# Performance work log

Hardware: AMD Instinct MI355X
Metric: run time of the kernel (lower is better)

## Reference

```python
import jax, jax.numpy as jnp
import numpy as np

B, T, DIM, H, BUCKET = 4, 4096, 1024, 16, 64
E = DIM // H          # head dim = 64
U = T // BUCKET       # number of buckets = 64
EPS = 1e-6


def setup_inputs() -> dict:
    key = jax.random.key(0)
    ks = jax.random.split(key, 5)
    scale = 1.0 / np.sqrt(DIM)
    return {
        "x": jax.random.normal(ks[0], (B, T, DIM), dtype=jnp.float32),
        "Wq": jax.random.normal(ks[1], (DIM, DIM), dtype=jnp.float32) * scale,
        "Wk": jax.random.normal(ks[2], (DIM, DIM), dtype=jnp.float32) * scale,
        "Wv": jax.random.normal(ks[3], (DIM, DIM), dtype=jnp.float32) * scale,
        "Wo": jax.random.normal(ks[4], (DIM, DIM), dtype=jnp.float32) * scale,
        "bo": jnp.zeros((DIM,), dtype=jnp.float32),
    }


def _causal_linear_attn(q, k, v):
    # q, k, v: [b, h, t, e]; psi(k) = elu(k) + 1; q softmaxed over feature dim
    q = jax.nn.softmax(q, axis=-1)
    k = jax.nn.elu(k) + 1.0
    bucket = lambda x: x.reshape(*x.shape[:-2], U, BUCKET, E)  # [b,h,u,n,e]
    b_q, b_k, b_v = bucket(q), bucket(k), bucket(v)
    # cumulative key sums per bucket: [b,h,u,d]
    b_k_cumsum = jnp.cumsum(b_k.sum(axis=-2), axis=2)
    # per-bucket context then cumulative over buckets: [b,h,u,d,e]
    context = jnp.einsum("bhund,bhune->bhude", b_k, b_v)
    context = jnp.cumsum(context, axis=2)
    context = context / (b_k_cumsum[..., None] + EPS)
    # shift by one bucket (blindspot): bucket u sees context through bucket u-1
    context = jnp.concatenate(
        [jnp.zeros_like(context[:, :, :1]), context[:, :, :-1]], axis=2
    )
    attn = jnp.einsum("bhund,bhude->bhune", b_q, context)
    return attn.reshape(q.shape)  # [b,h,t,e]


def reference(x, Wq, Wk, Wv, Wo, bo):
    b, t, _ = x.shape
    q = x @ Wq
    k = x @ Wk
    v = x @ Wv
    merge = lambda z: z.reshape(b, t, H, E).transpose(0, 2, 1, 3)  # [b,h,t,e]
    attn = _causal_linear_attn(merge(q), merge(k), merge(v))
    out = attn.transpose(0, 2, 1, 3).reshape(b, t, DIM)
    return out @ Wo + bo
```

## Files before the change

### kernel.cpp

```cpp
#include <hip/hip_runtime.h>


#define T_LEN 4096
#define DIMN  1024
#define NHEAD 16
#define NB    4
#define MROWS (NB * T_LEN)

typedef float f32x4 __attribute__((ext_vector_type(4)));
typedef short s16x8 __attribute__((ext_vector_type(8)));
typedef short s16x4 __attribute__((ext_vector_type(4)));
using u16 = unsigned short;

__device__ __forceinline__ u16 f2bf(float f) {
  unsigned int u = __float_as_uint(f);
  u += 0x7fffu + ((u >> 16) & 1u);
  return (u16)(u >> 16);
}
__device__ __forceinline__ float bf2f(u16 h) {
  return __uint_as_float(((unsigned int)h) << 16);
}
__device__ __forceinline__ int swz16k(int off) {
  return off ^ (((off >> 7) & 3) << 4);
}

__global__ __launch_bounds__(256) void cvt_all_kern(const float* __restrict__ x,
                                                    const float* __restrict__ W0,
                                                    const float* __restrict__ W1,
                                                    const float* __restrict__ W2,
                                                    const float* __restrict__ W3,
                                                    u16* __restrict__ WT,
                                                    u16* __restrict__ xb) {
  __shared__ float tile[64][65];
  const int tid = threadIdx.x;
  if (blockIdx.x < 1024) {
    const int blk = blockIdx.x & 255;
    const int sel = blockIdx.x >> 8;
    const float* W = (sel == 0) ? W0 : (sel == 1) ? W1 : (sel == 2) ? W2 : W3;
    u16* dst = WT + (size_t)sel * DIMN * DIMN;
    const int k0 = (blk >> 4) << 6;
    const int n0 = (blk & 15) << 6;
    const int r = tid >> 6;
    const int c = tid & 63;
#pragma unroll
    for (int i = 0; i < 16; ++i) {
      int row = (i << 2) + r;
      tile[row][c] = W[(size_t)(k0 + row) * DIMN + n0 + c];
    }
    __syncthreads();
#pragma unroll
    for (int i = 0; i < 16; ++i) {
      int row = (i << 2) + r;
      dst[(size_t)(n0 + row) * DIMN + k0 + c] = f2bf(tile[c][row]);
    }
  } else {
    size_t i = ((size_t)(blockIdx.x - 1024) * 256 + tid) * 4;
    f32x4 v = *(const f32x4*)(x + i);
    s16x4 o;
    o.x = (short)f2bf(v.x); o.y = (short)f2bf(v.y);
    o.z = (short)f2bf(v.z); o.w = (short)f2bf(v.w);
    *(s16x4*)(xb + i) = o;
  }
}

__global__ __launch_bounds__(512, 4) void gemm_qkv(
    const u16* __restrict__ A, const u16* __restrict__ Bt,
    u16* __restrict__ dq, u16* __restrict__ dk, u16* __restrict__ dv) {
  constexpr int K = 1024;
  constexpr int BNT = 12;
  constexpr int NT = K / 32;
  __shared__ char lds[73728];

  const int tid = threadIdx.x;
  const int l = tid & 63;
  const int w = tid >> 6;
  const int wm = w >> 2;
  const int wn = w & 3;

  const int xcd = (int)blockIdx.x & 7;
  const int idx = (int)blockIdx.x >> 3;
  const int g = idx / (4 * BNT);
  const int r2 = idx % (4 * BNT);
  const int bn = r2 >> 2;
  const int bm = xcd * 16 + g * 4 + (r2 & 3);
  const size_t arow0 = (size_t)bm * 128;
  const size_t brow0 = (size_t)bn * 256;

  int lrow[2], lcol[2];
#pragma unroll
  for (int i = 0; i < 2; ++i) {
    int lg2 = swz16k((i * 512 + tid) * 16);
    lrow[i] = lg2 >> 6;
    lcol[i] = (lg2 & 63) >> 1;
  }

  const int fr = l & 15;
  const int kswz = (((l >> 4) << 4)) ^ ((((fr >> 1) & 3)) << 4);

  auto STAGE = [&](int buf, int matsel, int tt) {
    const int kbase = (tt & (NT - 1)) * 32;
#pragma unroll
    for (int i = 0; i < 2; ++i) {
      if (matsel == 0 && i == 1) break;
      const u16* src = (matsel == 0)
          ? A  + (arow0 + (size_t)lrow[i]) * K + kbase + lcol[i]
          : Bt + (brow0 + (size_t)lrow[i]) * K + kbase + lcol[i];
      char* dst = lds + (buf * 24576 + matsel * 8192 + (i * 512 + tid) * 16);
      __builtin_amdgcn_global_load_lds(
          (__attribute__((address_space(1))) const void*)src,
          (__attribute__((address_space(3))) void*)dst, 16, 0, 0);
    }
  };
  auto LDA = [&](int buf, int rowb) -> s16x8 {
    return *(const s16x8*)(lds + buf * 24576 + rowb * 64 + kswz);
  };
  auto LDB = [&](int buf, int rowb) -> s16x8 {
    return *(const s16x8*)(lds + buf * 24576 + 8192 + rowb * 64 + kswz);
  };

  f32x4 acc[4][4];
#pragma unroll
  for (int i = 0; i < 4; ++i)
#pragma unroll
    for (int j = 0; j < 4; ++j) acc[i][j] = {0.f, 0.f, 0.f, 0.f};

  STAGE(0, 0, 0); STAGE(0, 1, 0);
  STAGE(1, 0, 1); STAGE(1, 1, 1);
  asm volatile("s_waitcnt vmcnt(3)" ::: "memory");
  __builtin_amdgcn_sched_barrier(0);
  __builtin_amdgcn_s_barrier();

  const int amb = wm * 64;
  const int bnb = wn * 64;
  s16x8 af[4], bf[4];

  int bufR = 0, bufW = 2;
#pragma unroll 1
  for (int t = 0; t < NT; ++t) {
    STAGE(bufW, 0, t + 2);
    STAGE(bufW, 1, t + 2);
#pragma unroll
    for (int i = 0; i < 4; ++i) af[i] = LDA(bufR, amb + i * 16 + fr);
#pragma unroll
    for (int i = 0; i < 4; ++i) bf[i] = LDB(bufR, bnb + i * 16 + fr);
    __builtin_amdgcn_s_setprio(1);
#pragma unroll
    for (int mi = 0; mi < 4; ++mi)
#pragma unroll
      for (int ni = 0; ni < 4; ++ni)
        acc[mi][ni] = __builtin_amdgcn_mfma_f32_16x16x32_bf16(
            af[mi], bf[ni], acc[mi][ni], 0, 0, 0);
    __builtin_amdgcn_s_setprio(0);
    asm volatile("s_waitcnt vmcnt(3)" ::: "memory");
    __builtin_amdgcn_sched_barrier(0);
    __builtin_amdgcn_s_barrier();
    bufR = (bufR == 2) ? 0 : bufR + 1;
    bufW = (bufW == 2) ? 0 : bufW + 1;
  }

  asm volatile("s_waitcnt vmcnt(0) lgkmcnt(0)" ::: "memory");
  __builtin_amdgcn_sched_barrier(0);
  __builtin_amdgcn_s_barrier();

  const int r0 = (l >> 4) << 2;
  const int c0 = l & 15;
  const int mat = bn >> 2;
  if (mat == 0) {
    u16* dst = dq;
    const size_t colbase = (size_t)(bn & 3) * 256 + (size_t)wn * 64;
#pragma unroll
    for (int mi = 0; mi < 4; ++mi) {
#pragma unroll
      for (int j = 0; j < 4; ++j) {
        float v0 = acc[mi][0][j], v1 = acc[mi][1][j];
        float v2 = acc[mi][2][j], v3 = acc[mi][3][j];
        float m = fmaxf(fmaxf(v0, v1), fmaxf(v2, v3));
#pragma unroll
        for (int off = 1; off < 16; off <<= 1) m = fmaxf(m, __shfl_xor(m, off));
        float e0 = __expf(v0 - m), e1 = __expf(v1 - m);
        float e2 = __expf(v2 - m), e3 = __expf(v3 - m);
        float s = e0 + e1 + e2 + e3;
#pragma unroll
        for (int off = 1; off < 16; off <<= 1) s += __shfl_xor(s, off);
        float inv = 1.f / s;
        const size_t row = arow0 + wm * 64 + mi * 16 + r0 + j;
        u16* p = dst + row * DIMN + colbase + c0;
        p[0]  = f2bf(e0 * inv); p[16] = f2bf(e1 * inv);
        p[32] = f2bf(e2 * inv); p[48] = f2bf(e3 * inv);
      }
    }
  } else {
    u16* dst = (mat == 1) ? dk : dv;
    u16* lt = (u16*)lds;
#pragma unroll
    for (int mi = 0; mi < 4; ++mi) {
      const int tl = wm * 64 + mi * 16 + r0;
#pragma unroll
      for (int ni = 0; ni < 4; ++ni) {
        const int cl = wn * 64 + ni * 16 + c0;
        s16x4 o;
#pragma unroll
        for (int j = 0; j < 4; ++j) {
          float v = acc[mi][ni][j];
          float r = (mat == 1) ? (v > 0.f ? v + 1.f : __expf(v)) : v;
          o[j] = (short)f2bf(r);
        }
        *(s16x4*)&lt[cl * 132 + tl] = o;
      }
    }
    __builtin_amdgcn_s_barrier();
    const int colb = (bn & 3) * 256;
    const int bb = (int)(arow0 >> 12);
    const int t0 = (int)(arow0 & 4095);
#pragma unroll
    for (int i = 0; i < 8; ++i) {
      const int chunk = i * 512 + tid;
      const int cl = chunk >> 4;
      const int toct = (chunk & 15) * 8;
      s16x8 vv = *(const s16x8*)&lt[cl * 132 + toct];
      const int col = colb + cl;
      const int h = col >> 6, d = col & 63;
      *(s16x8*)&dst[((size_t)((bb * 16 + h) * 64 + d)) * 4096 + t0 + toct] = vv;
    }
  }
}

__global__ __launch_bounds__(512, 2) void gemm_o(
    const u16* __restrict__ A, const u16* __restrict__ Bt,
    float* __restrict__ dO, const float* __restrict__ bias) {
  constexpr int K = 1024;
  constexpr int NT = K / 32;
  extern __shared__ char lds[];

  const int tid = threadIdx.x;
  const int l = tid & 63;
  const int w = tid >> 6;
  const int wm = w >> 2;
  const int wn = w & 3;

  const int xcd = (int)blockIdx.x & 7;
  const int idx = (int)blockIdx.x >> 3;
  const int bm = xcd * 16 + (idx & 15);
  const int bn = idx >> 4;
  const size_t arow0 = (size_t)bm * 128;
  const size_t brow0 = (size_t)bn * 512;

  int lrowA, lcolA, lrowB[4], lcolB[4];
  {
    int lg2 = swz16k(tid * 16);
    lrowA = lg2 >> 6; lcolA = (lg2 & 63) >> 1;
#pragma unroll
    for (int i = 0; i < 4; ++i) {
      int lb = swz16k((i * 512 + tid) * 16);
      lrowB[i] = lb >> 6; lcolB[i] = (lb & 63) >> 1;
    }
  }

  const int fr = l & 15;
  const int kswz = (((l >> 4) << 4)) ^ ((((fr >> 1) & 3)) << 4);

  auto STAGE = [&](int buf, int tt) {
    const int kbase = (tt & (NT - 1)) * 32;
    {
      const u16* src = A + (arow0 + (size_t)lrowA) * K + kbase + lcolA;
      char* dst = lds + (buf * 40960 + tid * 16);
      __builtin_amdgcn_global_load_lds(
          (__attribute__((address_space(1))) const void*)src,
          (__attribute__((address_space(3))) void*)dst, 16, 0, 0);
    }
#pragma unroll
    for (int i = 0; i < 4; ++i) {
      const u16* src = Bt + (brow0 + (size_t)lrowB[i]) * K + kbase + lcolB[i];
      char* dst = lds + (buf * 40960 + 8192 + (i * 512 + tid) * 16);
      __builtin_amdgcn_global_load_lds(
          (__attribute__((address_space(1))) const void*)src,
          (__attribute__((address_space(3))) void*)dst, 16, 0, 0);
    }
  };
  auto LDA = [&](int buf, int rowb) -> s16x8 {
    return *(const s16x8*)(lds + buf * 40960 + rowb * 64 + kswz);
  };
  auto LDB = [&](int buf, int rowb) -> s16x8 {
    return *(const s16x8*)(lds + buf * 40960 + 8192 + rowb * 64 + kswz);
  };

  f32x4 acc[4][8];
#pragma unroll
  for (int i = 0; i < 4; ++i)
#pragma unroll
    for (int j = 0; j < 8; ++j) acc[i][j] = {0.f, 0.f, 0.f, 0.f};

  STAGE(0, 0);
  STAGE(1, 1);
  asm volatile("s_waitcnt vmcnt(5)" ::: "memory");
  __builtin_amdgcn_sched_barrier(0);
  __builtin_amdgcn_s_barrier();

  const int amb = wm * 64;
  const int bnb = wn * 128;
  s16x8 af[4], bf[8];

  int bufR = 0, bufW = 2;
#pragma unroll 1
  for (int t = 0; t < NT; ++t) {
    STAGE(bufW, t + 2);
#pragma unroll
    for (int i = 0; i < 4; ++i) af[i] = LDA(bufR, amb + i * 16 + fr);
#pragma unroll
    for (int i = 0; i < 8; ++i) bf[i] = LDB(bufR, bnb + i * 16 + fr);
    __builtin_amdgcn_s_setprio(1);
#pragma unroll
    for (int mi = 0; mi < 4; ++mi)
#pragma unroll
      for (int ni = 0; ni < 8; ++ni)
        acc[mi][ni] = __builtin_amdgcn_mfma_f32_16x16x32_bf16(
            af[mi], bf[ni], acc[mi][ni], 0, 0, 0);
    __builtin_amdgcn_s_setprio(0);
    asm volatile("s_waitcnt vmcnt(5)" ::: "memory");
    __builtin_amdgcn_sched_barrier(0);
    __builtin_amdgcn_s_barrier();
    bufR = (bufR == 2) ? 0 : bufR + 1;
    bufW = (bufW == 2) ? 0 : bufW + 1;
  }

  const int r0 = (l >> 4) << 2;
  const int c0 = l & 15;
#pragma unroll
  for (int mi = 0; mi < 4; ++mi)
#pragma unroll
    for (int ni = 0; ni < 8; ++ni) {
      const size_t col = brow0 + (size_t)wn * 128 + ni * 16 + c0;
      const float bv = bias[col];
#pragma unroll
      for (int j = 0; j < 4; ++j) {
        const size_t row = arow0 + wm * 64 + mi * 16 + r0 + j;
        dO[row * DIMN + col] = acc[mi][ni][j] + bv;
      }
    }
}

__global__ __launch_bounds__(512) void mid_fused_kern(const u16* __restrict__ kT,
                                                      const u16* __restrict__ vT,
                                                      const u16* __restrict__ qb,
                                                      u16* __restrict__ attn) {
  __shared__ u16 cprev[2][16][72];
  const int tid = threadIdx.x;
  const int l = tid & 63;
  const int w = tid >> 6;
  const int ws = w & 3;
  const bool isCtx = w < 4;
  const int fr = l & 15;
  const int lg = l >> 4;

  const int bid = (int)blockIdx.x;
  const int xcd = bid & 7;
  const int slot = bid >> 3;
  const int bh = xcd * 8 + (slot >> 2);
  const int eg = slot & 3;
  const int b = bh >> 4, h = bh & 15;

  const size_t kvbase = (size_t)bh * 64 * 4096;
  const size_t qrow0 = (size_t)b * T_LEN;

  if (isCtx) {
#pragma unroll
    for (int j = 0; j < 4; ++j) cprev[0][lg * 4 + j][ws * 16 + fr] = 0;
  }
  __syncthreads();

  if (isCtx) {
    auto LV = [&](int u, int kk) -> s16x8 {
      return *(const s16x8*)&vT[kvbase + (size_t)(eg * 16 + fr) * 4096 +
                                u * 64 + kk * 32 + lg * 8];
    };
    auto LK = [&](int u, int kk) -> s16x8 {
      return *(const s16x8*)&kT[kvbase + (size_t)(ws * 16 + fr) * 4096 +
                                u * 64 + kk * 32 + lg * 8];
    };
    f32x4 cacc = {0.f, 0.f, 0.f, 0.f};
    float ksum = 0.f;
    s16x8 vA0 = LV(0, 0), vA1 = LV(0, 1);
    s16x8 kB0 = LK(0, 0), kB1 = LK(0, 1);
#pragma unroll 1
    for (int u = 0; u < 64; ++u) {
      const s16x8 cvA0 = vA0, cvA1 = vA1, ckB0 = kB0, ckB1 = kB1;
      if (u < 63) {
        vA0 = LV(u + 1, 0); vA1 = LV(u + 1, 1);
        kB0 = LK(u + 1, 0); kB1 = LK(u + 1, 1);
      }
      cacc = __builtin_amdgcn_mfma_f32_16x16x32_bf16(cvA0, ckB0, cacc, 0, 0, 0);
      cacc = __builtin_amdgcn_mfma_f32_16x16x32_bf16(cvA1, ckB1, cacc, 0, 0, 0);
      float s = 0.f;
#pragma unroll
      for (int j = 0; j < 8; ++j)
        s += bf2f((u16)ckB0[j]) + bf2f((u16)ckB1[j]);
      s += __shfl_xor(s, 16);
      s += __shfl_xor(s, 32);
      ksum += s;
      const float inv = 1.f / (ksum + 1e-6f);
      u16* pp = &cprev[(u + 1) & 1][lg * 4][ws * 16 + fr];
#pragma unroll
      for (int j = 0; j < 4; ++j) pp[j * 72] = f2bf(cacc[j] * inv);
      __syncthreads();
    }
  } else {
    auto LQ = [&](int u, int kk) -> s16x8 {
      return *(const s16x8*)&qb[(qrow0 + u * 64 + ws * 16 + fr) * DIMN +
                                (size_t)h * 64 + kk * 32 + lg * 8];
    };
    s16x8 qA0 = LQ(0, 0), qA1 = LQ(0, 1);
#pragma unroll 1
    for (int u = 0; u < 64; ++u) {
      const s16x8 cqA0 = qA0, cqA1 = qA1;
      if (u < 63) { qA0 = LQ(u + 1, 0); qA1 = LQ(u + 1, 1); }
      s16x8 cB0 = *(const s16x8*)&cprev[u & 1][fr][lg * 8];
      s16x8 cB1 = *(const s16x8*)&cprev[u & 1][fr][32 + lg * 8];
      f32x4 aacc = {0.f, 0.f, 0.f, 0.f};
      aacc = __builtin_amdgcn_mfma_f32_16x16x32_bf16(cqA0, cB0, aacc, 0, 0, 0);
      aacc = __builtin_amdgcn_mfma_f32_16x16x32_bf16(cqA1, cB1, aacc, 0, 0, 0);
      const size_t arow = qrow0 + (size_t)u * 64 + ws * 16 + lg * 4;
#pragma unroll
      for (int j = 0; j < 4; ++j)
        attn[(arow + j) * DIMN + (size_t)h * 64 + eg * 16 + fr] = f2bf(aacc[j]);
      __syncthreads();
    }
  }
}

extern "C" void kernel_launch(void* const* d_in, const int* in_sizes, int n_in,
                              void* d_out, int out_size, void* d_ws, size_t ws_size,
                              hipStream_t stream) {
  const float* x  = (const float*)d_in[0];
  const float* Wq = (const float*)d_in[1];
  const float* Wk = (const float*)d_in[2];
  const float* Wv = (const float*)d_in[3];
  const float* Wo = (const float*)d_in[4];
  const float* bo = (const float*)d_in[5];
  float* out = (float*)d_out;

  constexpr size_t SZ_XB = (size_t)MROWS * DIMN * 2;
  constexpr size_t SZ_WT = (size_t)DIMN * DIMN * 2;
  char* ws = (char*)d_ws;
  u16*   xb   = (u16*)(ws);
  u16*   wqT  = (u16*)(ws + SZ_XB);
  u16*   woT  = (u16*)(ws + SZ_XB + 3 * SZ_WT);
  u16*   qb   = (u16*)(ws + SZ_XB + 4 * SZ_WT);
  u16*   kT   = (u16*)(ws + 2 * SZ_XB + 4 * SZ_WT);
  u16*   vT   = (u16*)(ws + 3 * SZ_XB + 4 * SZ_WT);
  u16*   attn = xb;

  (void)hipFuncSetAttribute((const void*)gemm_o,
                            hipFuncAttributeMaxDynamicSharedMemorySize, 122880);

  cvt_all_kern<<<1024 + MROWS * DIMN / 1024, 256, 0, stream>>>(x, Wq, Wk, Wv, Wo,
                                                               wqT, xb);

  gemm_qkv<<<1536, 512, 0, stream>>>(xb, wqT, qb, kT, vT);

  mid_fused_kern<<<256, 512, 0, stream>>>(kT, vT, qb, attn);

  gemm_o<<<256, 512, 122880, stream>>>(attn, woT, out, bo);
}
```

Measured before the change: 245.2 us.

## Batch four buckets per barrier in fused context/query stage with 8-slot LDS ring

The producer warps (context accumulation) now handle four buckets between barriers and write the prefix contexts into an 8-slot shared ring. The consumer warps run one group behind, reading those four slots. This cuts the number of block-wide barriers from 64 to 17 and deepens the prefetch of K/V/Q loads to four buckets. The cost is more registers for the deeper prefetch, slightly more LDS, and a one-group lag between the two warp roles. The explicit zero-init of slot 0 is dropped, since the producer now writes the zero context before its first MFMA.

```diff
diff --git a/kernel.cpp b/kernel.cpp
--- a/kernel.cpp
+++ b/kernel.cpp
@@ -343,7 +343,7 @@
                                                       const u16* __restrict__ vT,
                                                       const u16* __restrict__ qb,
                                                       u16* __restrict__ attn) {
-  __shared__ u16 cprev[2][16][72];
+  __shared__ u16 cprev[8][16][72];
   const int tid = threadIdx.x;
   const int l = tid & 63;
   const int w = tid >> 6;
@@ -361,12 +361,6 @@
 
   const size_t kvbase = (size_t)bh * 64 * 4096;
   const size_t qrow0 = (size_t)b * T_LEN;
-
-  if (isCtx) {
-#pragma unroll
-    for (int j = 0; j < 4; ++j) cprev[0][lg * 4 + j][ws * 16 + fr] = 0;
-  }
-  __syncthreads();
 
   if (isCtx) {
     auto LV = [&](int u, int kk) -> s16x8 {
@@ -379,28 +373,53 @@
     };
     f32x4 cacc = {0.f, 0.f, 0.f, 0.f};
     float ksum = 0.f;
-    s16x8 vA0 = LV(0, 0), vA1 = LV(0, 1);
-    s16x8 kB0 = LK(0, 0), kB1 = LK(0, 1);
+    s16x8 vA[4][2], kB[4][2];
+#pragma unroll
+    for (int s = 0; s < 4; ++s)
+#pragma unroll
+      for (int kk = 0; kk < 2; ++kk) {
+        vA[s][kk] = LV(s, kk);
+        kB[s][kk] = LK(s, kk);
+      }
 #pragma unroll 1
-    for (int u = 0; u < 64; ++u) {
-      const s16x8 cvA0 = vA0, cvA1 = vA1, ckB0 = kB0, ckB1 = kB1;
-      if (u < 63) {
-        vA0 = LV(u + 1, 0); vA1 = LV(u + 1, 1);
-        kB0 = LK(u + 1, 0); kB1 = LK(u + 1, 1);
+    for (int t = 0; t <= 16; ++t) {
+      if (t < 16) {
+        s16x8 a[4][2], b2[4][2];
+#pragma unroll
+        for (int s = 0; s < 4; ++s)
+#pragma unroll
+          for (int kk = 0; kk < 2; ++kk) {
+            a[s][kk] = vA[s][kk];
+            b2[s][kk] = kB[s][kk];
+          }
+        if (t < 15) {
+#pragma unroll
+          for (int s = 0; s < 4; ++s)
+#pragma unroll
+            for (int kk = 0; kk < 2; ++kk) {
+              vA[s][kk] = LV(4 * t + 4 + s, kk);
+              kB[s][kk] = LK(4 * t + 4 + s, kk);
+            }
+        }
+#pragma unroll
+        for (int s = 0; s < 4; ++s) {
+          const float inv = 1.f / (ksum + 1e-6f);
+          u16* pp = &cprev[(4 * t + s) & 7][lg * 4][ws * 16 + fr];
+#pragma unroll
+          for (int j = 0; j < 4; ++j) pp[j * 72] = f2bf(cacc[j] * inv);
+          cacc = __builtin_amdgcn_mfma_f32_16x16x32_bf16(a[s][0], b2[s][0],
+                                                         cacc, 0, 0, 0);
+          cacc = __builtin_amdgcn_mfma_f32_16x16x32_bf16(a[s][1], b2[s][1],
+                                                         cacc, 0, 0, 0);
+          float ss = 0.f;
+#pragma unroll
+          for (int j = 0; j < 8; ++j)
+            ss += bf2f((u16)b2[s][0][j]) + bf2f((u16)b2[s][1][j]);
+          ss += __shfl_xor(ss, 16);
+          ss += __shfl_xor(ss, 32);
+          ksum += ss;
+        }
       }
-      cacc = __builtin_amdgcn_mfma_f32_16x16x32_bf16(cvA0, ckB0, cacc, 0, 0, 0);
-      cacc = __builtin_amdgcn_mfma_f32_16x16x32_bf16(cvA1, ckB1, cacc, 0, 0, 0);
-      float s = 0.f;
-#pragma unroll
-      for (int j = 0; j < 8; ++j)
-        s += bf2f((u16)ckB0[j]) + bf2f((u16)ckB1[j]);
-      s += __shfl_xor(s, 16);
-      s += __shfl_xor(s, 32);
-      ksum += s;
-      const float inv = 1.f / (ksum + 1e-6f);
-      u16* pp = &cprev[(u + 1) & 1][lg * 4][ws * 16 + fr];
-#pragma unroll
-      for (int j = 0; j < 4; ++j) pp[j * 72] = f2bf(cacc[j] * inv);
       __syncthreads();
     }
   } else {
@@ -408,20 +427,42 @@
       return *(const s16x8*)&qb[(qrow0 + u * 64 + ws * 16 + fr) * DIMN +
                                 (size_t)h * 64 + kk * 32 + lg * 8];
     };
-    s16x8 qA0 = LQ(0, 0), qA1 = LQ(0, 1);
+    s16x8 qA[4][2];
+#pragma unroll
+    for (int s = 0; s < 4; ++s)
+#pragma unroll
+      for (int kk = 0; kk < 2; ++kk) qA[s][kk] = LQ(s, kk);
 #pragma unroll 1
-    for (int u = 0; u < 64; ++u) {
-      const s16x8 cqA0 = qA0, cqA1 = qA1;
-      if (u < 63) { qA0 = LQ(u + 1, 0); qA1 = LQ(u + 1, 1); }
-      s16x8 cB0 = *(const s16x8*)&cprev[u & 1][fr][lg * 8];
-      s16x8 cB1 = *(const s16x8*)&cprev[u & 1][fr][32 + lg * 8];
-      f32x4 aacc = {0.f, 0.f, 0.f, 0.f};
-      aacc = __builtin_amdgcn_mfma_f32_16x16x32_bf16(cqA0, cB0, aacc, 0, 0, 0);
-      aacc = __builtin_amdgcn_mfma_f32_16x16x32_bf16(cqA1, cB1, aacc, 0, 0, 0);
-      const size_t arow = qrow0 + (size_t)u * 64 + ws * 16 + lg * 4;
-#pragma unroll
-      for (int j = 0; j < 4; ++j)
-        attn[(arow + j) * DIMN + (size_t)h * 64 + eg * 16 + fr] = f2bf(aacc[j]);
+    for (int t = 0; t <= 16; ++t) {
+      if (t >= 1) {
+        s16x8 c[4][2];
+#pragma unroll
+        for (int s = 0; s < 4; ++s)
+#pragma unroll
+          for (int kk = 0; kk < 2; ++kk) c[s][kk] = qA[s][kk];
+        if (t < 16) {
+#pragma unroll
+          for (int s = 0; s < 4; ++s)
+#pragma unroll
+            for (int kk = 0; kk < 2; ++kk) qA[s][kk] = LQ(4 * t + s, kk);
+        }
+#pragma unroll
+        for (int s = 0; s < 4; ++s) {
+          const int u = 4 * (t - 1) + s;
+          s16x8 cB0 = *(const s16x8*)&cprev[u & 7][fr][lg * 8];
+          s16x8 cB1 = *(const s16x8*)&cprev[u & 7][fr][32 + lg * 8];
+          f32x4 aacc = {0.f, 0.f, 0.f, 0.f};
+          aacc = __builtin_amdgcn_mfma_f32_16x16x32_bf16(c[s][0], cB0, aacc,
+                                                         0, 0, 0);
+          aacc = __builtin_amdgcn_mfma_f32_16x16x32_bf16(c[s][1], cB1, aacc,
+                                                         0, 0, 0);
+          const size_t arow = qrow0 + (size_t)u * 64 + ws * 16 + lg * 4;
+#pragma unroll
+          for (int j = 0; j < 4; ++j)
+            attn[(arow + j) * DIMN + (size_t)h * 64 + eg * 16 + fr] =
+                f2bf(aacc[j]);
+        }
+      }
       __syncthreads();
     }
   }
```

After: 235.4 us. 1.04x faster.
